# Performance work log

Measured on AMD Instinct MI355X. Metric: run time of the kernel, lower is better.

The kernel has to match this reference:

```python
import jax, jax.numpy as jnp
import numpy as np

N = 50000      # nodes
E = 800000     # edges (before self-loops)
IN = 256       # in_channels
HID = 64       # hidden_channels per head
HEADS = 8
OUT = 64       # out_channels
NEG_SLOPE = 0.2  # PyG GATConv leaky_relu slope


def gat_conv(x, W, a_src, a_dst, b, src, dst, heads, outc, concat):
    # x: [n, f_in]; W: [f_in, heads*outc]; a_src/a_dst: [heads, outc]; b: bias
    n = x.shape[0]
    h = (x @ W).reshape(n, heads, outc)                      # [n, H, C]
    alpha_s = (h * a_src).sum(-1)                            # [n, H]
    alpha_d = (h * a_dst).sum(-1)                            # [n, H]
    e = jax.nn.leaky_relu(alpha_s[src] + alpha_d[dst], NEG_SLOPE)  # [E, H]
    # segment softmax over destination node
    m = jax.lax.stop_gradient(jax.ops.segment_max(e, dst, num_segments=n))
    ex = jnp.exp(e - m[dst])                                 # [E, H]
    den = jax.ops.segment_sum(ex, dst, num_segments=n)       # [n, H]
    alpha = ex / (den[dst] + 1e-16)                          # [E, H]
    out = jax.ops.segment_sum(alpha[..., None] * h[src], dst, num_segments=n)  # [n, H, C]
    out = out.reshape(n, heads * outc) if concat else out.mean(axis=1)
    return out + b


def setup_inputs() -> dict:
    key = jax.random.key(0)
    ks = jax.random.split(key, 10)
    s = 0.1
    return {
        "x": jax.random.normal(ks[0], (N, IN), jnp.float32),
        "edge_index": jax.random.randint(ks[1], (2, E), 0, N, dtype=jnp.int64)
            if jax.config.jax_enable_x64 else jax.random.randint(ks[1], (2, E), 0, N, dtype=jnp.int32),
        "W1": jax.random.normal(ks[2], (IN, HEADS * HID), jnp.float32) * s,
        "a_src1": jax.random.normal(ks[3], (HEADS, HID), jnp.float32) * s,
        "a_dst1": jax.random.normal(ks[4], (HEADS, HID), jnp.float32) * s,
        "b1": jnp.zeros((HEADS * HID,), jnp.float32),
        "W2": jax.random.normal(ks[5], (HEADS * HID, OUT), jnp.float32) * s,
        "a_src2": jax.random.normal(ks[6], (1, OUT), jnp.float32) * s,
        "a_dst2": jax.random.normal(ks[7], (1, OUT), jnp.float32) * s,
        "b2": jnp.zeros((OUT,), jnp.float32),
    }


def reference(x, W1, a_src1, a_dst1, b1, W2, a_src2, a_dst2, b2, edge_index):
    # eval mode: dropout is identity. PyG GATConv adds self-loops by default.
    loop = jnp.arange(N, dtype=edge_index.dtype)
    src = jnp.concatenate([edge_index[0], loop])
    dst = jnp.concatenate([edge_index[1], loop])
    h = jax.nn.elu(gat_conv(x, W1, a_src1, a_dst1, b1, src, dst, HEADS, HID, True))
    return gat_conv(h, W2, a_src2, a_dst2, b2, src, dst, 1, OUT, False)
```

## Files before the change

kernel.cpp:

```cpp
#include <hip/hip_runtime.h>
#include <cstddef>

#define NN   50000
#define EE   800000
#define TOTE 850000
#define INC  256
#define HEADS 8
#define F1   512
#define OUTC 64
#define NB   ((NN + 255) / 256)

#define PB_CVTX   ((NN * INC / 8 + 255) / 256)
#define PB_CVTW1  ((INC * F1 + 255) / 256)
#define PB_CVTW2  ((F1 * OUTC + 255) / 256)
#define PB_COUNT  ((TOTE + 255) / 256)

typedef unsigned short ushort_t;
typedef unsigned int uint_t;
typedef __attribute__((ext_vector_type(8))) short short8;
typedef __attribute__((ext_vector_type(4))) float f32x4;

__device__ __forceinline__ ushort_t f32_to_bf16_rne(float f) {
  uint_t u = __float_as_uint(f);
  u += 0x7fffu + ((u >> 16) & 1u);
  return (ushort_t)(u >> 16);
}
__device__ __forceinline__ float bf16lo_to_f32(uint_t u) {
  return __uint_as_float(u << 16);
}
__device__ __forceinline__ float bf16hi_to_f32(uint_t u) {
  return __uint_as_float(u & 0xffff0000u);
}
__device__ __forceinline__ float lrelu(float x) { return fmaxf(x, 0.2f * x); }

__device__ __forceinline__ void gload16(const ushort_t* g, ushort_t* l) {
  __builtin_amdgcn_global_load_lds(
      (const __attribute__((address_space(1))) void*)g,
      (__attribute__((address_space(3))) void*)l, 16, 0, 0);
}

__global__ __launch_bounds__(256)
void prelude_kernel(const float* __restrict__ x, ushort_t* __restrict__ xbf,
                    const float* __restrict__ W1, ushort_t* __restrict__ W1T,
                    const float* __restrict__ W2, ushort_t* __restrict__ W2T,
                    const int* __restrict__ dsts, int* __restrict__ deg) {
  int b = blockIdx.x;
  if (b < PB_CVTX) {
    long i = ((long)b * 256 + threadIdx.x) * 8;
    if (i >= (long)NN * INC) return;
    float4 v0 = *reinterpret_cast<const float4*>(x + i);
    float4 v1 = *reinterpret_cast<const float4*>(x + i + 4);
    ushort_t p[8] = {f32_to_bf16_rne(v0.x), f32_to_bf16_rne(v0.y),
                     f32_to_bf16_rne(v0.z), f32_to_bf16_rne(v0.w),
                     f32_to_bf16_rne(v1.x), f32_to_bf16_rne(v1.y),
                     f32_to_bf16_rne(v1.z), f32_to_bf16_rne(v1.w)};
    *reinterpret_cast<uint4*>(xbf + i) = *reinterpret_cast<uint4*>(p);
    return;
  }
  b -= PB_CVTX;
  if (b < PB_CVTW1) {
    int i = b * 256 + threadIdx.x;
    if (i >= INC * F1) return;
    int k = i / F1, n = i % F1;
    W1T[(size_t)n * INC + k] = f32_to_bf16_rne(W1[i]);
    return;
  }
  b -= PB_CVTW1;
  if (b < PB_CVTW2) {
    int i = b * 256 + threadIdx.x;
    if (i >= F1 * OUTC) return;
    int k = i / OUTC, n = i % OUTC;
    W2T[(size_t)n * F1 + k] = f32_to_bf16_rne(W2[i]);
    return;
  }
  b -= PB_CVTW2;
  {
    int e = b * 256 + threadIdx.x;
    if (e >= TOTE) return;
    int dst = (e < EE) ? dsts[e] : (e - EE);
    atomicAdd(&deg[dst], 1);
  }
}

__global__ __launch_bounds__(256, 2)
void gemm_mfma(const ushort_t* __restrict__ A, const ushort_t* __restrict__ BT,
               const float* __restrict__ a_src, const float* __restrict__ a_dst,
               ushort_t* __restrict__ Cbf, float* __restrict__ AS,
               float* __restrict__ AD, int M, int K, int Nn, int nheads) {
  __shared__ __align__(16) ushort_t sA[128 * 64];
  __shared__ __align__(16) ushort_t sB[64 * 64];
  const int tid = threadIdx.x;
  const int w = tid >> 6, lane = tid & 63;

  int p = blockIdx.x;
  int nwg = gridDim.x;
  int l = ((nwg & 7) == 0) ? ((p & 7) * (nwg >> 3) + (p >> 3)) : p;
  const int rowBase = (l / nheads) * 128;
  const int head = l % nheads;
  const int colBase = head * 64;

  const int l8 = lane >> 3;
  const int srcslot = (lane & 7) ^ l8;
  size_t aOff[4]; ushort_t* aLds[4];
  #pragma unroll
  for (int q = 0; q < 4; ++q) {
    int r0 = w * 32 + q * 8;
    int grow = rowBase + r0 + l8; if (grow > M - 1) grow = M - 1;
    aOff[q] = (size_t)grow * K + srcslot * 8;
    aLds[q] = sA + r0 * 64;
  }
  size_t bOff[2]; ushort_t* bLds[2];
  #pragma unroll
  for (int q = 0; q < 2; ++q) {
    int c0 = w * 16 + q * 8;
    bOff[q] = (size_t)(colBase + c0 + l8) * K + srcslot * 8;
    bLds[q] = sB + c0 * 64;
  }

  f32x4 acc[2][4];
  #pragma unroll
  for (int mf = 0; mf < 2; ++mf)
    #pragma unroll
    for (int cf = 0; cf < 4; ++cf)
      acc[mf][cf] = (f32x4){0.f, 0.f, 0.f, 0.f};

  const int nkt = K >> 6;
  for (int kt = 0; kt < nkt; ++kt) {
    __syncthreads();
    #pragma unroll
    for (int q = 0; q < 4; ++q) gload16(A + aOff[q] + kt * 64, aLds[q]);
    #pragma unroll
    for (int q = 0; q < 2; ++q) gload16(BT + bOff[q] + kt * 64, bLds[q]);
    __syncthreads();
    #pragma unroll
    for (int ks = 0; ks < 2; ++ks) {
      const int sl = ks * 4 + (lane >> 4);
      short8 af[2], bfr[4];
      #pragma unroll
      for (int mf = 0; mf < 2; ++mf) {
        int row = w * 32 + mf * 16 + (lane & 15);
        af[mf] = *reinterpret_cast<short8*>((char*)sA + row * 128 + ((sl ^ (row & 7)) << 4));
      }
      #pragma unroll
      for (int cf = 0; cf < 4; ++cf) {
        int col = cf * 16 + (lane & 15);
        bfr[cf] = *reinterpret_cast<short8*>((char*)sB + col * 128 + ((sl ^ (col & 7)) << 4));
      }
      #pragma unroll
      for (int mf = 0; mf < 2; ++mf)
        #pragma unroll
        for (int cf = 0; cf < 4; ++cf)
          acc[mf][cf] = __builtin_amdgcn_mfma_f32_16x16x32_bf16(af[mf], bfr[cf], acc[mf][cf], 0, 0, 0);
    }
  }

  const int g = lane >> 4, c = lane & 15;
  float asv[4], adv[4];
  #pragma unroll
  for (int cf = 0; cf < 4; ++cf) {
    asv[cf] = a_src[colBase + cf * 16 + c];
    adv[cf] = a_dst[colBase + cf * 16 + c];
  }
  #pragma unroll
  for (int mf = 0; mf < 2; ++mf) {
    #pragma unroll
    for (int r = 0; r < 4; ++r) {
      int row = rowBase + w * 32 + mf * 16 + g * 4 + r;
      bool ok = row < M;
      float s = 0.f, d = 0.f;
      #pragma unroll
      for (int cf = 0; cf < 4; ++cf) {
        float v = acc[mf][cf][r];
        s = fmaf(v, asv[cf], s);
        d = fmaf(v, adv[cf], d);
        if (ok) Cbf[(size_t)row * Nn + colBase + cf * 16 + c] = f32_to_bf16_rne(v);
      }
      #pragma unroll
      for (int off = 8; off > 0; off >>= 1) {
        s += __shfl_xor(s, off);
        d += __shfl_xor(d, off);
      }
      if (ok && c == 0) {
        AS[(size_t)row * nheads + head] = s;
        AD[(size_t)row * nheads + head] = d;
      }
    }
  }
}

__global__ __launch_bounds__(256)
void scanA_kernel(const int* __restrict__ deg, int* __restrict__ rowptr,
                  int* __restrict__ psum) {
  __shared__ int sh[256];
  int t = threadIdx.x;
  int i = blockIdx.x * 256 + t;
  int v = (i < NN) ? deg[i] : 0;
  sh[t] = v;
  __syncthreads();
  #pragma unroll
  for (int off = 1; off < 256; off <<= 1) {
    int t2 = (t >= off) ? sh[t - off] : 0;
    __syncthreads();
    sh[t] += t2;
    __syncthreads();
  }
  if (i < NN) rowptr[i + 1] = sh[t];
  if (t == 255) psum[blockIdx.x] = sh[255];
}

__global__ __launch_bounds__(256)
void scanC_kernel(int* __restrict__ rowptr, const int* __restrict__ psum) {
  __shared__ int sh[256];
  int t = threadIdx.x;
  int v = (t < NB) ? psum[t] : 0;
  sh[t] = v;
  __syncthreads();
  #pragma unroll
  for (int off = 1; off < 256; off <<= 1) {
    int t2 = (t >= off) ? sh[t - off] : 0;
    __syncthreads();
    sh[t] += t2;
    __syncthreads();
  }
  int base = (blockIdx.x > 0) ? sh[blockIdx.x - 1] : 0;
  int i = blockIdx.x * 256 + t;
  if (i < NN) rowptr[i + 1] += base;
  if (i == 0) rowptr[0] = 0;
}

__global__ __launch_bounds__(256)
void scatter_kernel(const int* __restrict__ srcs, const int* __restrict__ dsts,
                    const int* __restrict__ rowptr, int* __restrict__ cursor,
                    int* __restrict__ esrc) {
  int e = blockIdx.x * blockDim.x + threadIdx.x;
  if (e >= TOTE) return;
  int src, dst;
  if (e < EE) { src = srcs[e]; dst = dsts[e]; }
  else        { src = e - EE;  dst = e - EE; }
  int pos = rowptr[dst] + atomicAdd(&cursor[dst], 1);
  esrc[pos] = src;
}

__global__ __launch_bounds__(256)
void agg1_kernel(const ushort_t* __restrict__ H1bf, const float* __restrict__ AS,
                 const float* __restrict__ AD, const int* __restrict__ rowptr,
                 const int* __restrict__ esrc, const float* __restrict__ b1,
                 ushort_t* __restrict__ OUT) {
  int n = (blockIdx.x * blockDim.x + threadIdx.x) >> 6;
  int lane = threadIdx.x & 63;
  if (n >= NN) return;
  int off = lane * 8;
  int h = lane >> 3;
  float ad = AD[n * HEADS + h];
  int s0 = rowptr[n], s1 = rowptr[n + 1];
  float den = 0.f;
  float a0 = 0.f, a1 = 0.f, a2 = 0.f, a3 = 0.f, a4 = 0.f, a5 = 0.f, a6 = 0.f, a7 = 0.f;
  int j = s0;
  for (; j + 1 < s1; j += 2) {
    int srcA = esrc[j], srcB = esrc[j + 1];
    float asA = AS[srcA * HEADS + h];
    float asB = AS[srcB * HEADS + h];
    uint4 vA = *reinterpret_cast<const uint4*>(H1bf + (size_t)srcA * F1 + off);
    uint4 vB = *reinterpret_cast<const uint4*>(H1bf + (size_t)srcB * F1 + off);
    float wA = __expf(lrelu(asA + ad));
    float wB = __expf(lrelu(asB + ad));
    den += wA + wB;
    a0 = fmaf(wA, bf16lo_to_f32(vA.x), a0); a0 = fmaf(wB, bf16lo_to_f32(vB.x), a0);
    a1 = fmaf(wA, bf16hi_to_f32(vA.x), a1); a1 = fmaf(wB, bf16hi_to_f32(vB.x), a1);
    a2 = fmaf(wA, bf16lo_to_f32(vA.y), a2); a2 = fmaf(wB, bf16lo_to_f32(vB.y), a2);
    a3 = fmaf(wA, bf16hi_to_f32(vA.y), a3); a3 = fmaf(wB, bf16hi_to_f32(vB.y), a3);
    a4 = fmaf(wA, bf16lo_to_f32(vA.z), a4); a4 = fmaf(wB, bf16lo_to_f32(vB.z), a4);
    a5 = fmaf(wA, bf16hi_to_f32(vA.z), a5); a5 = fmaf(wB, bf16hi_to_f32(vB.z), a5);
    a6 = fmaf(wA, bf16lo_to_f32(vA.w), a6); a6 = fmaf(wB, bf16lo_to_f32(vB.w), a6);
    a7 = fmaf(wA, bf16hi_to_f32(vA.w), a7); a7 = fmaf(wB, bf16hi_to_f32(vB.w), a7);
  }
  if (j < s1) {
    int srcA = esrc[j];
    float asA = AS[srcA * HEADS + h];
    uint4 vA = *reinterpret_cast<const uint4*>(H1bf + (size_t)srcA * F1 + off);
    float wA = __expf(lrelu(asA + ad));
    den += wA;
    a0 = fmaf(wA, bf16lo_to_f32(vA.x), a0);
    a1 = fmaf(wA, bf16hi_to_f32(vA.x), a1);
    a2 = fmaf(wA, bf16lo_to_f32(vA.y), a2);
    a3 = fmaf(wA, bf16hi_to_f32(vA.y), a3);
    a4 = fmaf(wA, bf16lo_to_f32(vA.z), a4);
    a5 = fmaf(wA, bf16hi_to_f32(vA.z), a5);
    a6 = fmaf(wA, bf16lo_to_f32(vA.w), a6);
    a7 = fmaf(wA, bf16hi_to_f32(vA.w), a7);
  }
  float rden = 1.f / (den + 1e-16f);
  float4 b_lo = *reinterpret_cast<const float4*>(b1 + off);
  float4 b_hi = *reinterpret_cast<const float4*>(b1 + off + 4);
  float r[8];
  r[0] = fmaf(a0, rden, b_lo.x); r[1] = fmaf(a1, rden, b_lo.y);
  r[2] = fmaf(a2, rden, b_lo.z); r[3] = fmaf(a3, rden, b_lo.w);
  r[4] = fmaf(a4, rden, b_hi.x); r[5] = fmaf(a5, rden, b_hi.y);
  r[6] = fmaf(a6, rden, b_hi.z); r[7] = fmaf(a7, rden, b_hi.w);
  ushort_t pk[8];
  #pragma unroll
  for (int i = 0; i < 8; ++i) {
    float e = r[i] > 0.f ? r[i] : expm1f(r[i]);
    pk[i] = f32_to_bf16_rne(e);
  }
  *reinterpret_cast<uint4*>(OUT + (size_t)n * F1 + off) = *reinterpret_cast<uint4*>(pk);
}

__global__ __launch_bounds__(256)
void agg2_kernel(const ushort_t* __restrict__ H2bf, const float* __restrict__ AS,
                 const float* __restrict__ AD, const int* __restrict__ rowptr,
                 const int* __restrict__ esrc, const float* __restrict__ b2,
                 float* __restrict__ OUT) {
  int n = (blockIdx.x * blockDim.x + threadIdx.x) >> 6;
  int lane = threadIdx.x & 63;
  if (n >= NN) return;
  int grp = lane >> 3;
  int c8 = (lane & 7) * 8;
  float ad = AD[n];
  int s0 = rowptr[n], s1 = rowptr[n + 1];
  float den = 0.f;
  float a0 = 0.f, a1 = 0.f, a2 = 0.f, a3 = 0.f, a4 = 0.f, a5 = 0.f, a6 = 0.f, a7 = 0.f;
  for (int j0 = s0; j0 < s1; j0 += 8) {
    int j = j0 + grp;
    bool valid = j < s1;
    int src = esrc[valid ? j : s0];
    float as = AS[src];
    uint4 v = *reinterpret_cast<const uint4*>(H2bf + (size_t)src * OUTC + c8);
    float w = valid ? __expf(lrelu(as + ad)) : 0.f;
    den += w;
    a0 = fmaf(w, bf16lo_to_f32(v.x), a0);
    a1 = fmaf(w, bf16hi_to_f32(v.x), a1);
    a2 = fmaf(w, bf16lo_to_f32(v.y), a2);
    a3 = fmaf(w, bf16hi_to_f32(v.y), a3);
    a4 = fmaf(w, bf16lo_to_f32(v.z), a4);
    a5 = fmaf(w, bf16hi_to_f32(v.z), a5);
    a6 = fmaf(w, bf16lo_to_f32(v.w), a6);
    a7 = fmaf(w, bf16hi_to_f32(v.w), a7);
  }
  #pragma unroll
  for (int st = 8; st < 64; st <<= 1) {
    den += __shfl_xor(den, st);
    a0 += __shfl_xor(a0, st); a1 += __shfl_xor(a1, st);
    a2 += __shfl_xor(a2, st); a3 += __shfl_xor(a3, st);
    a4 += __shfl_xor(a4, st); a5 += __shfl_xor(a5, st);
    a6 += __shfl_xor(a6, st); a7 += __shfl_xor(a7, st);
  }
  if (grp == 0) {
    float rden = 1.f / (den + 1e-16f);
    float4 o0, o1;
    o0.x = fmaf(a0, rden, b2[c8 + 0]); o0.y = fmaf(a1, rden, b2[c8 + 1]);
    o0.z = fmaf(a2, rden, b2[c8 + 2]); o0.w = fmaf(a3, rden, b2[c8 + 3]);
    o1.x = fmaf(a4, rden, b2[c8 + 4]); o1.y = fmaf(a5, rden, b2[c8 + 5]);
    o1.z = fmaf(a6, rden, b2[c8 + 6]); o1.w = fmaf(a7, rden, b2[c8 + 7]);
    *reinterpret_cast<float4*>(OUT + (size_t)n * OUTC + c8) = o0;
    *reinterpret_cast<float4*>(OUT + (size_t)n * OUTC + c8 + 4) = o1;
  }
}

extern "C" void kernel_launch(void* const* d_in, const int* in_sizes, int n_in,
                              void* d_out, int out_size, void* d_ws, size_t ws_size,
                              hipStream_t stream) {
  const float* x      = (const float*)d_in[0];
  const int*   edges  = (const int*)d_in[1];
  const float* W1     = (const float*)d_in[2];
  const float* a_src1 = (const float*)d_in[3];
  const float* a_dst1 = (const float*)d_in[4];
  const float* b1     = (const float*)d_in[5];
  const float* W2     = (const float*)d_in[6];
  const float* a_src2 = (const float*)d_in[7];
  const float* a_dst2 = (const float*)d_in[8];
  const float* b2     = (const float*)d_in[9];
  float* out = (float*)d_out;

  const int* srcs = edges;
  const int* dsts = edges + EE;

  float* AS1    = (float*)d_ws;
  float* AD1    = AS1    + (size_t)NN * HEADS;
  float* AS2    = AD1    + (size_t)NN * HEADS;
  float* AD2    = AS2    + NN;
  ushort_t* xbf   = (ushort_t*)(AD2 + NN);
  ushort_t* W1T   = xbf  + (size_t)NN * INC;
  ushort_t* W2T   = W1T  + (size_t)F1 * INC;
  ushort_t* H1bf  = W2T  + (size_t)OUTC * F1;
  ushort_t* AG1bf = H1bf + (size_t)NN * F1;
  ushort_t* H2bf  = AG1bf + (size_t)NN * F1;
  int* deg    = (int*)(H2bf + (size_t)NN * OUTC);
  int* rowptr = deg + NN;
  int* cursor = rowptr + NN + 1;
  int* psum   = cursor + NN;
  int* esrc   = psum + NB;

  hipMemsetAsync(deg, 0, (size_t)(3 * NN + 1) * sizeof(int), stream);

  prelude_kernel<<<PB_CVTX + PB_CVTW1 + PB_CVTW2 + PB_COUNT, 256, 0, stream>>>(
      x, xbf, W1, W1T, W2, W2T, dsts, deg);

  scanA_kernel<<<NB, 256, 0, stream>>>(deg, rowptr, psum);
  scanC_kernel<<<NB, 256, 0, stream>>>(rowptr, psum);
  scatter_kernel<<<(TOTE + 255) / 256, 256, 0, stream>>>(srcs, dsts, rowptr, cursor, esrc);

  gemm_mfma<<<((NN + 127) / 128) * HEADS, 256, 0, stream>>>(
      xbf, W1T, a_src1, a_dst1, H1bf, AS1, AD1, NN, INC, F1, HEADS);
  agg1_kernel<<<(NN * 64 + 255) / 256, 256, 0, stream>>>(H1bf, AS1, AD1, rowptr, esrc, b1, AG1bf);

  gemm_mfma<<<(NN + 127) / 128, 256, 0, stream>>>(
      AG1bf, W2T, a_src2, a_dst2, H2bf, AS2, AD2, NN, F1, OUTC, 1);
  agg2_kernel<<<(NN * 64 + 255) / 256, 256, 0, stream>>>(H2bf, AS2, AD2, rowptr, esrc, b2, out);
}
```

Measured before the change: 307.8 us.

## Use 128x128 output tiles for layer-1 GEMM and generalize XCD swizzle

Adds a gemm_mfma128 kernel where each workgroup computes a 128x128 tile (two heads), with each wave owning a 64x64 sub-tile, and uses it for the first-layer projection. A-tile loads are then shared across two heads, which halves A traffic and raises MFMA work per LDS read. The XCD block swizzle is also generalized so it handles grid sizes that are not multiples of 8, which now applies to the second GEMM too. In exchange it needs more accumulator registers per thread (64 floats), which may lower occupancy, and it launches fewer workgroups.

```diff
diff --git a/kernel.cpp b/kernel.cpp
--- a/kernel.cpp
+++ b/kernel.cpp
@@ -37,6 +37,11 @@
   __builtin_amdgcn_global_load_lds(
       (const __attribute__((address_space(1))) void*)g,
       (__attribute__((address_space(3))) void*)l, 16, 0, 0);
+}
+
+__device__ __forceinline__ int xcd_swz(int p, int nwg) {
+  int q = nwg >> 3, r = nwg & 7, x = p & 7;
+  return (x < r ? x * (q + 1) : r * (q + 1) + (x - r) * q) + (p >> 3);
 }
 
 __global__ __launch_bounds__(256)
@@ -83,6 +88,109 @@
 }
 
 __global__ __launch_bounds__(256, 2)
+void gemm_mfma128(const ushort_t* __restrict__ A, const ushort_t* __restrict__ BT,
+                  const float* __restrict__ a_src, const float* __restrict__ a_dst,
+                  ushort_t* __restrict__ Cbf, float* __restrict__ AS,
+                  float* __restrict__ AD, int M, int K, int Nn, int nheads) {
+  __shared__ __align__(16) ushort_t sA[128 * 64];
+  __shared__ __align__(16) ushort_t sB[128 * 64];
+  const int tid = threadIdx.x;
+  const int w = tid >> 6, lane = tid & 63;
+
+  const int l = xcd_swz(blockIdx.x, gridDim.x);
+  const int nColB = Nn >> 7;
+  const int rowBase = (l / nColB) * 128;
+  const int colBase = (l % nColB) * 128;
+
+  const int l8 = lane >> 3;
+  const int srcslot = (lane & 7) ^ l8;
+  size_t aOff[4]; ushort_t* aLds[4];
+  size_t bOff[4]; ushort_t* bLds[4];
+  #pragma unroll
+  for (int q = 0; q < 4; ++q) {
+    int r0 = w * 32 + q * 8;
+    int grow = rowBase + r0 + l8; if (grow > M - 1) grow = M - 1;
+    aOff[q] = (size_t)grow * K + srcslot * 8;
+    aLds[q] = sA + r0 * 64;
+    bOff[q] = (size_t)(colBase + r0 + l8) * K + srcslot * 8;
+    bLds[q] = sB + r0 * 64;
+  }
+
+  f32x4 acc[4][4];
+  #pragma unroll
+  for (int mf = 0; mf < 4; ++mf)
+    #pragma unroll
+    for (int cf = 0; cf < 4; ++cf)
+      acc[mf][cf] = (f32x4){0.f, 0.f, 0.f, 0.f};
+
+  const int wr = (w >> 1) * 64;
+  const int wc = (w & 1) * 64;
+  const int nkt = K >> 6;
+  for (int kt = 0; kt < nkt; ++kt) {
+    __syncthreads();
+    #pragma unroll
+    for (int q = 0; q < 4; ++q) gload16(A + aOff[q] + kt * 64, aLds[q]);
+    #pragma unroll
+    for (int q = 0; q < 4; ++q) gload16(BT + bOff[q] + kt * 64, bLds[q]);
+    __syncthreads();
+    #pragma unroll
+    for (int ks = 0; ks < 2; ++ks) {
+      const int sl = ks * 4 + (lane >> 4);
+      short8 af[4], bfr[4];
+      #pragma unroll
+      for (int mf = 0; mf < 4; ++mf) {
+        int row = wr + mf * 16 + (lane & 15);
+        af[mf] = *reinterpret_cast<short8*>((char*)sA + row * 128 + ((sl ^ (row & 7)) << 4));
+      }
+      #pragma unroll
+      for (int cf = 0; cf < 4; ++cf) {
+        int col = wc + cf * 16 + (lane & 15);
+        bfr[cf] = *reinterpret_cast<short8*>((char*)sB + col * 128 + ((sl ^ (col & 7)) << 4));
+      }
+      #pragma unroll
+      for (int mf = 0; mf < 4; ++mf)
+        #pragma unroll
+        for (int cf = 0; cf < 4; ++cf)
+          acc[mf][cf] = __builtin_amdgcn_mfma_f32_16x16x32_bf16(af[mf], bfr[cf], acc[mf][cf], 0, 0, 0);
+    }
+  }
+
+  const int g = lane >> 4, c = lane & 15;
+  const int head = (colBase + wc) >> 6;
+  float asv[4], adv[4];
+  #pragma unroll
+  for (int cf = 0; cf < 4; ++cf) {
+    asv[cf] = a_src[colBase + wc + cf * 16 + c];
+    adv[cf] = a_dst[colBase + wc + cf * 16 + c];
+  }
+  #pragma unroll
+  for (int mf = 0; mf < 4; ++mf) {
+    #pragma unroll
+    for (int r = 0; r < 4; ++r) {
+      int row = rowBase + wr + mf * 16 + g * 4 + r;
+      bool ok = row < M;
+      float s = 0.f, d = 0.f;
+      #pragma unroll
+      for (int cf = 0; cf < 4; ++cf) {
+        float v = acc[mf][cf][r];
+        s = fmaf(v, asv[cf], s);
+        d = fmaf(v, adv[cf], d);
+        if (ok) Cbf[(size_t)row * Nn + colBase + wc + cf * 16 + c] = f32_to_bf16_rne(v);
+      }
+      #pragma unroll
+      for (int off = 8; off > 0; off >>= 1) {
+        s += __shfl_xor(s, off);
+        d += __shfl_xor(d, off);
+      }
+      if (ok && c == 0) {
+        AS[(size_t)row * nheads + head] = s;
+        AD[(size_t)row * nheads + head] = d;
+      }
+    }
+  }
+}
+
+__global__ __launch_bounds__(256, 2)
 void gemm_mfma(const ushort_t* __restrict__ A, const ushort_t* __restrict__ BT,
                const float* __restrict__ a_src, const float* __restrict__ a_dst,
                ushort_t* __restrict__ Cbf, float* __restrict__ AS,
@@ -92,9 +200,7 @@
   const int tid = threadIdx.x;
   const int w = tid >> 6, lane = tid & 63;
 
-  int p = blockIdx.x;
-  int nwg = gridDim.x;
-  int l = ((nwg & 7) == 0) ? ((p & 7) * (nwg >> 3) + (p >> 3)) : p;
+  const int l = xcd_swz(blockIdx.x, gridDim.x);
   const int rowBase = (l / nheads) * 128;
   const int head = l % nheads;
   const int colBase = head * 64;
@@ -400,7 +506,7 @@
   scanC_kernel<<<NB, 256, 0, stream>>>(rowptr, psum);
   scatter_kernel<<<(TOTE + 255) / 256, 256, 0, stream>>>(srcs, dsts, rowptr, cursor, esrc);
 
-  gemm_mfma<<<((NN + 127) / 128) * HEADS, 256, 0, stream>>>(
+  gemm_mfma128<<<((NN + 127) / 128) * (F1 / 128), 256, 0, stream>>>(
       xbf, W1T, a_src1, a_dst1, H1bf, AS1, AD1, NN, INC, F1, HEADS);
   agg1_kernel<<<(NN * 64 + 255) / 256, 256, 0, stream>>>(H1bf, AS1, AD1, rowptr, esrc, b1, AG1bf);
 
```

After: 315.1 us. +2.4%, slower.
